# Performance work log

Hardware: AMD Instinct MI355X
Metric: run time of the kernel (lower is better)

Reference implementation:

```python
import jax, jax.numpy as jnp
import numpy as np

S = 2048      # sequence length
D = 2048      # d_model
H = 16        # n_heads
E = 128       # d_head


def setup_inputs() -> dict:
    key = jax.random.key(0)
    kx, kw = jax.random.split(key)
    x = jax.random.normal(kx, (S, D), dtype=jnp.float32)
    # xavier_normal for fan_in=D, fan_out=3*E per head
    std = float(np.sqrt(2.0 / (D + 3 * E)))
    w_qkv = jax.random.normal(kw, (H, D, 3 * E), dtype=jnp.float32) * std
    return {"x": x, "w_qkv": w_qkv}


def reference(x, w_qkv):
    # qkv: [h, s, 3e]
    qkv = jnp.einsum('sd,hde->hse', x, w_qkv)
    q, k, v = jnp.split(qkv, 3, axis=-1)            # each [h, s, e]
    scores = jnp.einsum('hse,hte->hst', q, k) / jnp.sqrt(jnp.asarray(E, x.dtype))
    attn = jax.nn.softmax(scores, axis=-1)          # [h, s, t]
    out = jnp.einsum('hst,hte->hse', attn, v)       # [h, s, e]
    # concat heads: [s, h*e]
    return out.transpose(1, 0, 2).reshape(x.shape[0], -1)
```

## Files before the change

### kernel.cpp

```cpp
#include <hip/hip_runtime.h>

#define SEQ 2048
#define DMODEL 2048
#define NHEAD 16
#define EHEAD 128
#define NE3 384

using short8 = __attribute__((ext_vector_type(8))) short;
using f32x4  = __attribute__((ext_vector_type(4))) float;
using f32x16 = __attribute__((ext_vector_type(16))) float;
using uint4v = __attribute__((ext_vector_type(4))) unsigned int;

__device__ __forceinline__ unsigned short f32_to_bf16(float f) {
    unsigned int u = __float_as_uint(f);
    unsigned int rounding = 0x7fffu + ((u >> 16) & 1u);
    u += rounding;
    return (unsigned short)(u >> 16);
}

__device__ __forceinline__ void async_load16(const void* g, void* l) {
    __builtin_amdgcn_global_load_lds(
        (const __attribute__((address_space(1))) unsigned int*)g,
        (__attribute__((address_space(3))) unsigned int*)l, 16, 0, 0);
}

#define WG_BARRIER()                              \
    do {                                          \
        asm volatile("" ::: "memory");            \
        __builtin_amdgcn_s_barrier();             \
        asm volatile("" ::: "memory");            \
    } while (0)

__global__ void cast_x_kernel(const float* __restrict__ x, unsigned short* __restrict__ xb) {
    int i = (blockIdx.x * blockDim.x + threadIdx.x) * 4;
    float4 v = *(const float4*)(x + i);
    ushort4 o = make_ushort4(f32_to_bf16(v.x), f32_to_bf16(v.y), f32_to_bf16(v.z), f32_to_bf16(v.w));
    *(ushort4*)(xb + i) = o;
}

__global__ void transpose_w_kernel(const float* __restrict__ w, unsigned short* __restrict__ wT) {
    __shared__ float tile[64][65];
    int h  = blockIdx.z;
    int d0 = blockIdx.x * 64;
    int n0 = blockIdx.y * 64;
    int t = threadIdx.x;
    int rr = t >> 4;
    int cc = (t & 15) * 4;
#pragma unroll
    for (int i = 0; i < 4; i++) {
        float4 v = *(const float4*)&w[(size_t)(h * DMODEL + d0 + rr + i * 16) * NE3 + n0 + cc];
        tile[rr + i * 16][cc + 0] = v.x;
        tile[rr + i * 16][cc + 1] = v.y;
        tile[rr + i * 16][cc + 2] = v.z;
        tile[rr + i * 16][cc + 3] = v.w;
    }
    __syncthreads();
#pragma unroll
    for (int i = 0; i < 4; i++) {
        int n = rr + i * 16;
        ushort4 o;
        o.x = f32_to_bf16(tile[cc + 0][n]);
        o.y = f32_to_bf16(tile[cc + 1][n]);
        o.z = f32_to_bf16(tile[cc + 2][n]);
        o.w = f32_to_bf16(tile[cc + 3][n]);
        *(ushort4*)&wT[(size_t)(h * NE3 + n0 + n) * DMODEL + d0 + cc] = o;
    }
}

template <int B, bool STAGE, int VM>
__device__ __forceinline__ void qkv_kstep(
        unsigned short* lds, f32x4 (&acc)[4][6],
        const unsigned short*& p0, const unsigned short*& p1,
        const unsigned short*& p2, const unsigned short*& p3,
        const int d0, const int d1, const int d2, const int d3,
        const int aoff, const int boff) {
    constexpr int B3 = ((B + 3) & 3) * 16384;
    const unsigned short* LA = lds + B * 16384 + aoff;
    const unsigned short* LB = lds + B * 16384 + boff;

    short8 a[4], b0[3];
#pragma unroll
    for (int mf = 0; mf < 4; ++mf) a[mf] = *(const short8*)(LA + mf * 512);
#pragma unroll
    for (int nf = 0; nf < 3; ++nf) b0[nf] = *(const short8*)(LB + nf * 512);
    if constexpr (STAGE) {
        async_load16(p0, lds + B3 + d0);
        async_load16(p1, lds + B3 + d1);
    }
    p0 += 32; p1 += 32;
    WG_BARRIER();
    __builtin_amdgcn_s_setprio(1);
#pragma unroll
    for (int mf = 0; mf < 4; ++mf)
#pragma unroll
        for (int nf = 0; nf < 3; ++nf)
            acc[mf][nf] = __builtin_amdgcn_mfma_f32_16x16x32_bf16(a[mf], b0[nf], acc[mf][nf], 0, 0, 0);
    __builtin_amdgcn_s_setprio(0);
    WG_BARRIER();

    short8 b1[3];
#pragma unroll
    for (int nf = 0; nf < 3; ++nf) b1[nf] = *(const short8*)(LB + (3 + nf) * 512);
    if constexpr (STAGE) {
        async_load16(p2, lds + B3 + d2);
        async_load16(p3, lds + B3 + d3);
    }
    p2 += 32; p3 += 32;
    if constexpr (VM == 8)      asm volatile("s_waitcnt vmcnt(8)" ::: "memory");
    else if constexpr (VM == 4) asm volatile("s_waitcnt vmcnt(4)" ::: "memory");
    else if constexpr (VM == 0) asm volatile("s_waitcnt vmcnt(0)" ::: "memory");
    WG_BARRIER();
    __builtin_amdgcn_s_setprio(1);
#pragma unroll
    for (int mf = 0; mf < 4; ++mf)
#pragma unroll
        for (int nf = 0; nf < 3; ++nf)
            acc[mf][3 + nf] = __builtin_amdgcn_mfma_f32_16x16x32_bf16(a[mf], b1[nf], acc[mf][3 + nf], 0, 0, 0);
    __builtin_amdgcn_s_setprio(0);
    WG_BARRIER();
}

__global__ __launch_bounds__(512, 2) void qkv_gemm384(
        const unsigned short* __restrict__ A,
        const unsigned short* __restrict__ Bm,
        unsigned short* __restrict__ Q,
        unsigned short* __restrict__ Kb,
        unsigned short* __restrict__ Vt) {
    extern __shared__ __attribute__((aligned(16))) unsigned short lds[];
    const int mb = blockIdx.x, nb = blockIdx.y;
    const int tid = threadIdx.x;
    const int wave = tid >> 6, lane = tid & 63;
    const int r = lane & 15, q = lane >> 4;
    const int wm = wave >> 2, wn = wave & 3;

    const int rrm  = (tid >> 2) & 15;
    const int kg   = ((tid & 3) ^ ((rrm >> 1) & 3)) * 8;
    const int rowA = ((tid >> 6) << 4) + rrm;
    const unsigned short* p0 = A  + (size_t)(mb * 128 + rowA) * DMODEL + kg;
    const unsigned short* p1 = Bm + (size_t)(nb * 384 + rowA) * DMODEL + kg;
    const unsigned short* p2 = p1 + (size_t)128 * DMODEL;
    const unsigned short* p3 = p1 + (size_t)256 * DMODEL;
    const int d0 = wave * 512;
    const int d1 = 4096 + wave * 512;
    const int d2 = 8192 + wave * 512;
    const int d3 = 12288 + wave * 512;

#pragma unroll
    for (int t = 0; t < 3; ++t) {
        async_load16(p0 + t * 32, lds + t * 16384 + d0);
        async_load16(p1 + t * 32, lds + t * 16384 + d1);
        async_load16(p2 + t * 32, lds + t * 16384 + d2);
        async_load16(p3 + t * 32, lds + t * 16384 + d3);
    }
    p0 += 96; p1 += 96; p2 += 96; p3 += 96;

    const int qs = q ^ ((r >> 1) & 3);
    const int aoff = wm * 2048 + r * 32 + qs * 8;
    const int boff = 4096 + wn * 3072 + r * 32 + qs * 8;

    f32x4 acc[4][6] = {};
    asm volatile("s_waitcnt vmcnt(8)" ::: "memory");
    WG_BARRIER();

    for (int i = 0; i < 15; ++i) {
        qkv_kstep<0, true, 8>(lds, acc, p0, p1, p2, p3, d0, d1, d2, d3, aoff, boff);
        qkv_kstep<1, true, 8>(lds, acc, p0, p1, p2, p3, d0, d1, d2, d3, aoff, boff);
        qkv_kstep<2, true, 8>(lds, acc, p0, p1, p2, p3, d0, d1, d2, d3, aoff, boff);
        qkv_kstep<3, true, 8>(lds, acc, p0, p1, p2, p3, d0, d1, d2, d3, aoff, boff);
    }
    qkv_kstep<0, true,  8>(lds, acc, p0, p1, p2, p3, d0, d1, d2, d3, aoff, boff);
    qkv_kstep<1, false, 4>(lds, acc, p0, p1, p2, p3, d0, d1, d2, d3, aoff, boff);
    qkv_kstep<2, false, 0>(lds, acc, p0, p1, p2, p3, d0, d1, d2, d3, aoff, boff);
    qkv_kstep<3, false, -1>(lds, acc, p0, p1, p2, p3, d0, d1, d2, d3, aoff, boff);

    const int head = nb;
    const int mbase = mb * 128 + wm * 64;
#pragma unroll
    for (int nf = 0; nf < 6; ++nf) {
        const int cb = wn * 96 + nf * 16;
        const int sel = cb >> 7;
        const int e = (cb & 127) + r;
#pragma unroll
        for (int mf = 0; mf < 4; ++mf) {
            const int row0 = mbase + mf * 16 + q * 4;
            const f32x4 v = acc[mf][nf];
            if (sel == 2) {
                ushort4 o;
                o.x = f32_to_bf16(v[0]);
                o.y = f32_to_bf16(v[1]);
                o.z = f32_to_bf16(v[2]);
                o.w = f32_to_bf16(v[3]);
                *(ushort4*)&Vt[((size_t)head * EHEAD + e) * SEQ + row0] = o;
            } else {
                unsigned short* dst = sel ? Kb : Q;
#pragma unroll
                for (int reg = 0; reg < 4; ++reg)
                    dst[((size_t)head * SEQ + row0 + reg) * EHEAD + e] = f32_to_bf16(v[reg]);
            }
        }
    }
}

__global__ __launch_bounds__(256, 2) void flash_attn(
        const unsigned short* __restrict__ Qg,
        const unsigned short* __restrict__ Kg,
        const unsigned short* __restrict__ Vtg,
        float* __restrict__ out) {
    extern __shared__ __attribute__((aligned(16))) unsigned short lds[];
    unsigned short* sQ  = lds;
    unsigned short* sK0 = lds + 8192;
    unsigned short* sV0 = lds + 24576;

    const int tid = threadIdx.x;
    const int wave = tid >> 6, lane = tid & 63;
    const int l31 = lane & 31, q2 = lane >> 5;
    const int wm = wave >> 1, wn = wave & 1;
    const int b = blockIdx.x;
    const int h  = (b & 7) + (((b >> 3) >> 5) << 3);
    const int m0 = ((b >> 3) & 31) * 64;

    const unsigned short* Qh  = Qg  + ((size_t)h * SEQ + m0) * EHEAD;
    const unsigned short* Kh0 = Kg  + (size_t)h * SEQ * EHEAD;
    const unsigned short* Vh  = Vtg + (size_t)h * EHEAD * SEQ;

    const int qkRow = lane >> 4;
    const int qkPos = lane & 15;
    const int vRow  = lane >> 3;
    const int vPos  = lane & 7;

    const unsigned short* gK[4];
    const unsigned short* gV[4];
#pragma unroll
    for (int c = 0; c < 4; c++) {
        int u = wave * 4 + c;
        int row = u * 4 + qkRow;
        int ch = qkPos ^ (row & 7);
        gK[c] = Kh0 + (size_t)row * EHEAD + ch * 8;
        int rv = u * 8 + vRow;
        int cv = vPos ^ (rv & 7);
        gV[c] = Vh + (size_t)rv * SEQ + cv * 8;
        async_load16(Qh + (size_t)row * EHEAD + ch * 8, sQ + u * 512);
        async_load16(gK[c], sK0 + u * 512);
        async_load16(gV[c], sV0 + u * 512);
        gK[c] += 64 * EHEAD;
        gV[c] += 64;
    }
    __syncthreads();

    short8 bq[8];
    {
        const int row = wm * 32 + l31;
#pragma unroll
        for (int kc = 0; kc < 8; kc++) {
            int p = (kc * 2 + q2) ^ (row & 7);
            bq[kc] = *(const short8*)&sQ[row * 128 + p * 8];
        }
    }

    const unsigned short* kp[8];
    const unsigned short* vp[8];
    const int rowA = wn * 32 + l31;
#pragma unroll
    for (int kc = 0; kc < 8; kc++)
        kp[kc] = sK0 + rowA * 128 + (((kc * 2 + q2) ^ (rowA & 7)) * 8);
#pragma unroll
    for (int et = 0; et < 4; et++)
#pragma unroll
        for (int kc2 = 0; kc2 < 2; kc2++) {
            int rowV = et * 32 + l31;
            int cch = wn * 4 + kc2 * 2 + q2;
            vp[et * 2 + kc2] = sV0 + rowV * 64 + ((cch ^ (rowV & 7)) * 8);
        }

    const float c1 = 0.12752405856f;
    f32x16 acc_o[4] = {};
    float l_acc = 0.f;

    auto body = [&](const int cur, const int nxt, bool pref) {
        if (pref) {
#pragma unroll
            for (int c = 0; c < 4; c++) {
                async_load16(gK[c], sK0 + nxt + (wave * 4 + c) * 512);
                gK[c] += 64 * EHEAD;
            }
#pragma unroll
            for (int c = 0; c < 4; c++) {
                async_load16(gV[c], sV0 + nxt + (wave * 4 + c) * 512);
                gV[c] += 64;
            }
        }

        f32x16 st = {};
#pragma unroll
        for (int kc = 0; kc < 8; kc++) {
            short8 ak = *(const short8*)(kp[kc] + cur);
            st = __builtin_amdgcn_mfma_f32_32x32x16_bf16(ak, bq[kc], st, 0, 0, 0);
        }

        unsigned int pk[8];
#pragma unroll
        for (int t = 0; t < 8; t++) {
            float p0 = __builtin_amdgcn_exp2f(st[2 * t] * c1);
            float p1 = __builtin_amdgcn_exp2f(st[2 * t + 1] * c1);
            l_acc += p0 + p1;
            unsigned int u0 = __float_as_uint(p0) + 0x8000u;
            unsigned int u1 = __float_as_uint(p1) + 0x8000u;
            pk[t] = __builtin_amdgcn_perm(u1, u0, 0x07060302u);
        }

        short8 fr[2];
#pragma unroll
        for (int kc2 = 0; kc2 < 2; kc2++) {
            unsigned int a0 = pk[kc2 * 4 + 0], a1 = pk[kc2 * 4 + 1];
            unsigned int a2 = pk[kc2 * 4 + 2], a3 = pk[kc2 * 4 + 3];
            unsigned int s0 = (unsigned int)__shfl_xor((int)a0, 32);
            unsigned int s1 = (unsigned int)__shfl_xor((int)a1, 32);
            unsigned int s2 = (unsigned int)__shfl_xor((int)a2, 32);
            unsigned int s3 = (unsigned int)__shfl_xor((int)a3, 32);
            uint4v t;
            t.x = q2 ? s2 : a0;
            t.y = q2 ? s3 : a1;
            t.z = q2 ? a2 : s0;
            t.w = q2 ? a3 : s1;
            fr[kc2] = __builtin_bit_cast(short8, t);
        }

#pragma unroll
        for (int et = 0; et < 4; et++)
#pragma unroll
            for (int kc2 = 0; kc2 < 2; kc2++) {
                short8 bv = *(const short8*)(vp[et * 2 + kc2] + cur);
                acc_o[et] = __builtin_amdgcn_mfma_f32_32x32x16_bf16(fr[kc2], bv, acc_o[et], 0, 0, 0);
            }
        __syncthreads();
    };

    for (int ip = 0; ip < SEQ / 128; ip++) {
        body(0, 8192, true);
        body(8192, 0, ip != SEQ / 128 - 1);
    }

    l_acc += __shfl_xor(l_acc, 32);

    float* fl = (float*)lds;
#pragma unroll
    for (int et = 0; et < 4; et++) {
        if ((et >> 1) != wn) {
#pragma unroll
            for (int rg = 0; rg < 4; rg++) {
                f32x4 v;
                v[0] = acc_o[et][rg * 4 + 0];
                v[1] = acc_o[et][rg * 4 + 1];
                v[2] = acc_o[et][rg * 4 + 2];
                v[3] = acc_o[et][rg * 4 + 3];
                *(f32x4*)&fl[(size_t)(((wm * 4 + et) * 4 + rg) * 256) + lane * 4] = v;
            }
        }
    }
    fl[8192 + (wm * 2 + wn) * 32 + l31] = l_acc;
    __syncthreads();

    float invq[4][4];
#pragma unroll
    for (int rg = 0; rg < 4; rg++)
#pragma unroll
        for (int i = 0; i < 4; i++) {
            int qy = i + 4 * q2 + 8 * rg;
            float lt = fl[8192 + (wm * 2 + 0) * 32 + qy] + fl[8192 + (wm * 2 + 1) * 32 + qy];
            invq[rg][i] = 1.0f / lt;
        }

#pragma unroll
    for (int et = 0; et < 4; et++) {
        if ((et >> 1) == wn) {
#pragma unroll
            for (int rg = 0; rg < 4; rg++) {
                f32x4 v = *(const f32x4*)&fl[(size_t)(((wm * 4 + et) * 4 + rg) * 256) + lane * 4];
#pragma unroll
                for (int i = 0; i < 4; i++) {
                    int mrow = i + 4 * q2 + 8 * rg;
                    out[(size_t)(m0 + wm * 32 + mrow) * DMODEL + h * EHEAD + et * 32 + l31] =
                        (acc_o[et][rg * 4 + i] + v[i]) * invq[rg][i];
                }
            }
        }
    }
}

extern "C" void kernel_launch(void* const* d_in, const int* in_sizes, int n_in,
                              void* d_out, int out_size, void* d_ws, size_t ws_size,
                              hipStream_t stream) {
    const float* x = (const float*)d_in[0];
    const float* w = (const float*)d_in[1];
    float* out = (float*)d_out;

    char* ws = (char*)d_ws;
    unsigned short* xb = (unsigned short*)(ws);
    unsigned short* wT = (unsigned short*)(ws + 8388608);
    unsigned short* Q  = (unsigned short*)(ws + 33554432);
    unsigned short* Kb = (unsigned short*)(ws + 41943040);
    unsigned short* Vt = (unsigned short*)(ws + 50331648);

    static bool attr_set = false;
    if (!attr_set) {
        hipFuncSetAttribute((const void*)flash_attn,
                            hipFuncAttributeMaxDynamicSharedMemorySize, 81920);
        hipFuncSetAttribute((const void*)qkv_gemm384,
                            hipFuncAttributeMaxDynamicSharedMemorySize, 131072);
        attr_set = true;
    }

    cast_x_kernel<<<SEQ * DMODEL / (256 * 4), 256, 0, stream>>>(x, xb);
    transpose_w_kernel<<<dim3(DMODEL / 64, NE3 / 64, NHEAD), 256, 0, stream>>>(w, wT);
    qkv_gemm384<<<dim3(SEQ / 128, NHEAD), 512, 131072, stream>>>(xb, wT, Q, Kb, Vt);
    flash_attn<<<512, 256, 81920, stream>>>(Q, Kb, Vt, out);
}
```

Measured before the change: 202.8 us.

## Prefetch next k-step LDS fragments into registers in QKV GEMM

The QKV projection GEMM now double-buffers its A/B register fragments, reading the next stage's LDS fragments after the first MFMA half so the LDS reads overlap compute instead of sitting at the start of each k-step. The vmcnt wait moves earlier and is relaxed to 6 outstanding loads, and the compiler memory clobbers around barriers are removed. This raises register pressure and removes the compiler fences, which could allow unsafe reordering of LDS accesses relative to barriers.

```diff
diff --git a/kernel.cpp b/kernel.cpp
--- a/kernel.cpp
+++ b/kernel.cpp
@@ -23,13 +23,6 @@
         (const __attribute__((address_space(1))) unsigned int*)g,
         (__attribute__((address_space(3))) unsigned int*)l, 16, 0, 0);
 }
-
-#define WG_BARRIER()                              \
-    do {                                          \
-        asm volatile("" ::: "memory");            \
-        __builtin_amdgcn_s_barrier();             \
-        asm volatile("" ::: "memory");            \
-    } while (0)
 
 __global__ void cast_x_kernel(const float* __restrict__ x, unsigned short* __restrict__ xb) {
     int i = (blockIdx.x * blockDim.x + threadIdx.x) * 4;
@@ -67,57 +60,60 @@
     }
 }
 
-template <int B, bool STAGE, int VM>
+template <int B, bool STAGE, int VM, bool RDNEXT>
 __device__ __forceinline__ void qkv_kstep(
         unsigned short* lds, f32x4 (&acc)[4][6],
+        short8 (&aC)[4], short8 (&bC)[3],
+        short8 (&aN)[4], short8 (&bN)[3],
         const unsigned short*& p0, const unsigned short*& p1,
         const unsigned short*& p2, const unsigned short*& p3,
         const int d0, const int d1, const int d2, const int d3,
         const int aoff, const int boff) {
-    constexpr int B3 = ((B + 3) & 3) * 16384;
-    const unsigned short* LA = lds + B * 16384 + aoff;
-    const unsigned short* LB = lds + B * 16384 + boff;
-
-    short8 a[4], b0[3];
-#pragma unroll
-    for (int mf = 0; mf < 4; ++mf) a[mf] = *(const short8*)(LA + mf * 512);
-#pragma unroll
-    for (int nf = 0; nf < 3; ++nf) b0[nf] = *(const short8*)(LB + nf * 512);
+    constexpr int CUR = B * 16384;
+    constexpr int NXT = ((B + 1) & 3) * 16384;
+    constexpr int DST = ((B + 3) & 3) * 16384;
+
+    short8 b1[3];
+#pragma unroll
+    for (int nf = 0; nf < 3; ++nf) b1[nf] = *(const short8*)(lds + CUR + boff + (3 + nf) * 512);
     if constexpr (STAGE) {
-        async_load16(p0, lds + B3 + d0);
-        async_load16(p1, lds + B3 + d1);
+        async_load16(p0, lds + DST + d0);
+        async_load16(p1, lds + DST + d1);
     }
     p0 += 32; p1 += 32;
-    WG_BARRIER();
+    if constexpr (VM == 6)      asm volatile("s_waitcnt vmcnt(6)");
+    else if constexpr (VM == 4) asm volatile("s_waitcnt vmcnt(4)");
+    else if constexpr (VM == 0) asm volatile("s_waitcnt vmcnt(0)");
+    __builtin_amdgcn_s_barrier();
     __builtin_amdgcn_s_setprio(1);
 #pragma unroll
     for (int mf = 0; mf < 4; ++mf)
 #pragma unroll
         for (int nf = 0; nf < 3; ++nf)
-            acc[mf][nf] = __builtin_amdgcn_mfma_f32_16x16x32_bf16(a[mf], b0[nf], acc[mf][nf], 0, 0, 0);
+            acc[mf][nf] = __builtin_amdgcn_mfma_f32_16x16x32_bf16(aC[mf], bC[nf], acc[mf][nf], 0, 0, 0);
     __builtin_amdgcn_s_setprio(0);
-    WG_BARRIER();
-
-    short8 b1[3];
-#pragma unroll
-    for (int nf = 0; nf < 3; ++nf) b1[nf] = *(const short8*)(LB + (3 + nf) * 512);
+    __builtin_amdgcn_s_barrier();
+
+    if constexpr (RDNEXT) {
+#pragma unroll
+        for (int mf = 0; mf < 4; ++mf) aN[mf] = *(const short8*)(lds + NXT + aoff + mf * 512);
+#pragma unroll
+        for (int nf = 0; nf < 3; ++nf) bN[nf] = *(const short8*)(lds + NXT + boff + nf * 512);
+    }
     if constexpr (STAGE) {
-        async_load16(p2, lds + B3 + d2);
-        async_load16(p3, lds + B3 + d3);
+        async_load16(p2, lds + DST + d2);
+        async_load16(p3, lds + DST + d3);
     }
     p2 += 32; p3 += 32;
-    if constexpr (VM == 8)      asm volatile("s_waitcnt vmcnt(8)" ::: "memory");
-    else if constexpr (VM == 4) asm volatile("s_waitcnt vmcnt(4)" ::: "memory");
-    else if constexpr (VM == 0) asm volatile("s_waitcnt vmcnt(0)" ::: "memory");
-    WG_BARRIER();
+    __builtin_amdgcn_s_barrier();
     __builtin_amdgcn_s_setprio(1);
 #pragma unroll
     for (int mf = 0; mf < 4; ++mf)
 #pragma unroll
         for (int nf = 0; nf < 3; ++nf)
-            acc[mf][3 + nf] = __builtin_amdgcn_mfma_f32_16x16x32_bf16(a[mf], b1[nf], acc[mf][3 + nf], 0, 0, 0);
+            acc[mf][3 + nf] = __builtin_amdgcn_mfma_f32_16x16x32_bf16(aC[mf], b1[nf], acc[mf][3 + nf], 0, 0, 0);
     __builtin_amdgcn_s_setprio(0);
-    WG_BARRIER();
+    __builtin_amdgcn_s_barrier();
 }
 
 __global__ __launch_bounds__(512, 2) void qkv_gemm384(
@@ -159,19 +155,25 @@
     const int boff = 4096 + wn * 3072 + r * 32 + qs * 8;
 
     f32x4 acc[4][6] = {};
-    asm volatile("s_waitcnt vmcnt(8)" ::: "memory");
-    WG_BARRIER();
+    asm volatile("s_waitcnt vmcnt(8)");
+    __builtin_amdgcn_s_barrier();
+
+    short8 aA[4], bA[3], aB[4], bB[3];
+#pragma unroll
+    for (int mf = 0; mf < 4; ++mf) aA[mf] = *(const short8*)(lds + aoff + mf * 512);
+#pragma unroll
+    for (int nf = 0; nf < 3; ++nf) bA[nf] = *(const short8*)(lds + boff + nf * 512);
 
     for (int i = 0; i < 15; ++i) {
-        qkv_kstep<0, true, 8>(lds, acc, p0, p1, p2, p3, d0, d1, d2, d3, aoff, boff);
-        qkv_kstep<1, true, 8>(lds, acc, p0, p1, p2, p3, d0, d1, d2, d3, aoff, boff);
-        qkv_kstep<2, true, 8>(lds, acc, p0, p1, p2, p3, d0, d1, d2, d3, aoff, boff);
-        qkv_kstep<3, true, 8>(lds, acc, p0, p1, p2, p3, d0, d1, d2, d3, aoff, boff);
-    }
-    qkv_kstep<0, true,  8>(lds, acc, p0, p1, p2, p3, d0, d1, d2, d3, aoff, boff);
-    qkv_kstep<1, false, 4>(lds, acc, p0, p1, p2, p3, d0, d1, d2, d3, aoff, boff);
-    qkv_kstep<2, false, 0>(lds, acc, p0, p1, p2, p3, d0, d1, d2, d3, aoff, boff);
-    qkv_kstep<3, false, -1>(lds, acc, p0, p1, p2, p3, d0, d1, d2, d3, aoff, boff);
+        qkv_kstep<0, true, 6, true>(lds, acc, aA, bA, aB, bB, p0, p1, p2, p3, d0, d1, d2, d3, aoff, boff);
+        qkv_kstep<1, true, 6, true>(lds, acc, aB, bB, aA, bA, p0, p1, p2, p3, d0, d1, d2, d3, aoff, boff);
+        qkv_kstep<2, true, 6, true>(lds, acc, aA, bA, aB, bB, p0, p1, p2, p3, d0, d1, d2, d3, aoff, boff);
+        qkv_kstep<3, true, 6, true>(lds, acc, aB, bB, aA, bA, p0, p1, p2, p3, d0, d1, d2, d3, aoff, boff);
+    }
+    qkv_kstep<0, true,  6, true >(lds, acc, aA, bA, aB, bB, p0, p1, p2, p3, d0, d1, d2, d3, aoff, boff);
+    qkv_kstep<1, false, 4, true >(lds, acc, aB, bB, aA, bA, p0, p1, p2, p3, d0, d1, d2, d3, aoff, boff);
+    qkv_kstep<2, false, 0, true >(lds, acc, aA, bA, aB, bB, p0, p1, p2, p3, d0, d1, d2, d3, aoff, boff);
+    qkv_kstep<3, false, -1, false>(lds, acc, aB, bB, aA, bA, p0, p1, p2, p3, d0, d1, d2, d3, aoff, boff);
 
     const int head = nb;
     const int mbase = mb * 128 + wm * 64;
```

Result: faster. 196.6 us (-3.0%).
